# Kernel optimization log

Measured on AMD Instinct MI355X. Metric: run time of the kernel, lower is better.

Reference implementation:

```python
import jax, jax.numpy as jnp
import numpy as np

B, T, N, D = 8, 24, 263, 512
N0, N1 = 32, 64
SEG = 12
LAMBDA_INIT = 0.8 - 0.6 * float(np.exp(-0.3 * (1 - 1)))  # layer_idx=1 -> 0.2


def _ln(x, g, b, eps=1e-5):
    m = jnp.mean(x, axis=-1, keepdims=True)
    v = jnp.var(x, axis=-1, keepdims=True)
    return (x - m) * jax.lax.rsqrt(v + eps) * g + b


def _proj(x, W):
    # 1x1 Conv2d over channel dim == per-position linear, W: [out, in]
    return jnp.einsum('btnd,ed->btne', x, W)


def _forward(x, agg_x0, agg_x1, tmp_map,
             Wq_s, Wk_s, Wv_s, lq1, lk1, lq2, lk2, ln_g, ln_b,
             Wq_a0, Wk_a0, Wv_a0, Wq_a1, Wk_a1, Wv_a1, M0, M1, Wagg, bagg,
             Wq_t, Wk_t, Wv_t, q_agg, Wk_tg, Wv_tg, Wout, bout):
    B, T, N, D = x.shape
    # ---- SpatialDiffAttn: spa_dim=256, heads=4, head_dim=32 (2*32 per head) ----
    H, dh = 4, 32
    q = _proj(x, Wq_s).reshape(B, T, N, H, 2 * dh)
    k = _proj(x, Wk_s).reshape(B, T, N, H, 2 * dh)
    v = _proj(x, Wv_s).reshape(B, T, N, H, 2 * dh)
    q1, q2 = q[..., :dh], q[..., dh:]
    k1, k2 = k[..., :dh], k[..., dh:]
    sc = dh ** -0.5
    # attn11/attn12 share softmax(q1 k1^T); cat([p1@v1, p1@v2]) == p1 @ v_full
    p1 = jax.nn.softmax(jnp.einsum('btnhd,btmhd->bthnm', q1, k1) * sc, axis=-1)
    a1 = jnp.einsum('bthnm,btmhe->btnhe', p1, v)
    p2 = jax.nn.softmax(jnp.einsum('btnhd,btmhd->bthnm', q2, k2) * sc, axis=-1)
    a2 = jnp.einsum('bthnm,btmhe->btnhe', p2, v)
    lam = jnp.exp(jnp.sum(lq1 * lk1)) - jnp.exp(jnp.sum(lq2 * lk2)) + LAMBDA_INIT
    s_x = (_ln(a1 - lam * a2, ln_g, ln_b) * (1.0 - LAMBDA_INIT)).reshape(B, T, N, H * 2 * dh)

    # ---- SpatialAttn aggregated branches (agg_dim=128, heads=2, head_dim=64) ----
    def agg_branch(ax, Wq, Wk, Wv, M):
        Ni = ax.shape[2]
        Ha, dha = 2, 64
        qa = _proj(ax, Wq).reshape(B, T, Ni, Ha, dha)
        ka = _proj(ax, Wk).reshape(B, T, Ni, Ha, dha)
        va = _proj(ax, Wv).reshape(B, T, Ni, Ha, dha)
        pa = jax.nn.softmax(jnp.einsum('btnhd,btmhd->bthnm', qa, ka) * (dha ** -0.5), axis=-1)
        sx = jnp.einsum('bthnm,btmhd->bthnd', pa, va)          # [B,T,Ha,Ni,dha]
        # cls_map = M^T -> pool Ni clusters up to N regions
        return jnp.einsum('mn,bthmd->btnhd', M, sx).reshape(B, T, N, Ha * dha)

    sg = agg_branch(agg_x0, Wq_a0, Wk_a0, Wv_a0, M0) + agg_branch(agg_x1, Wq_a1, Wk_a1, Wv_a1, M1)
    sg = sg @ Wagg.T + bagg

    # ---- TemporalAttn (tmp_dim=128, heads=2, head_dim=64) ----
    Ht, dht = 2, 64
    qt = _proj(x, Wq_t).reshape(B, T, N, Ht, dht)
    kt = _proj(x, Wk_t).reshape(B, T, N, Ht, dht)
    vt = _proj(x, Wv_t).reshape(B, T, N, Ht, dht)
    pt = jax.nn.softmax(jnp.einsum('btnhd,bsnhd->bnhts', qt, kt) * (dht ** -0.5), axis=-1)
    t_x = jnp.einsum('bnhts,bsnhd->btnhd', pt, vt).reshape(B, T, N, Ht * dht)

    # ---- TemporalAttn aggregated (learned query, seg_num=12) ----
    S = q_agg.shape[1]
    qg = q_agg.reshape(N, S, Ht, dht)
    kg = _proj(x, Wk_tg).reshape(B, T, N, Ht, dht)
    vg = _proj(x, Wv_tg).reshape(B, T, N, Ht, dht)
    pg = jax.nn.softmax(jnp.einsum('nshd,btnhd->bnhst', qg, kg) * (dht ** -0.5), axis=-1)
    tgx = jnp.einsum('bnhst,btnhd->bnshd', pg, vg).reshape(B, N, S, Ht * dht)
    tg = jnp.einsum('bnts,bnsd->btnd', tmp_map, tgx)           # [B,T,N,128]

    st = jnp.concatenate([s_x, sg, t_x, tg], axis=-1)          # [B,T,N,640]
    return st @ Wout.T + bout


def setup_inputs() -> dict:
    ks = jax.random.split(jax.random.key(0), 32)
    r = lambda i, shape, s=0.05: (jax.random.normal(ks[i], shape) * s).astype(jnp.float32)
    return dict(
        x=r(0, (B, T, N, D), 1.0),
        agg_x0=r(1, (B, T, N0, D), 1.0),
        agg_x1=r(2, (B, T, N1, D), 1.0),
        tmp_map=jax.random.uniform(ks[3], (B, N, T, SEG), dtype=jnp.float32),
        Wq_s=r(4, (256, D)), Wk_s=r(5, (256, D)), Wv_s=r(6, (256, D)),
        lq1=r(7, (32,), 0.1), lk1=r(8, (32,), 0.1), lq2=r(9, (32,), 0.1), lk2=r(10, (32,), 0.1),
        ln_g=jnp.ones((64,), jnp.float32), ln_b=jnp.zeros((64,), jnp.float32),
        Wq_a0=r(11, (128, D)), Wk_a0=r(12, (128, D)), Wv_a0=r(13, (128, D)),
        Wq_a1=r(14, (128, D)), Wk_a1=r(15, (128, D)), Wv_a1=r(16, (128, D)),
        M0=r(17, (N0, N), 0.1), M1=r(18, (N1, N), 0.1),
        Wagg=r(19, (128, 128)), bagg=jnp.zeros((128,), jnp.float32),
        Wq_t=r(20, (128, D)), Wk_t=r(21, (128, D)), Wv_t=r(22, (128, D)),
        q_agg=r(23, (N, SEG, 128), 1.0),
        Wk_tg=r(24, (128, D)), Wv_tg=r(25, (128, D)),
        Wout=r(26, (D, 640)), bout=jnp.zeros((D,), jnp.float32),
    )


def reference(x, agg_x0, agg_x1, tmp_map,
              Wq_s, Wk_s, Wv_s, lq1, lk1, lq2, lk2, ln_g, ln_b,
              Wq_a0, Wk_a0, Wv_a0, Wq_a1, Wk_a1, Wv_a1, M0, M1, Wagg, bagg,
              Wq_t, Wk_t, Wv_t, q_agg, Wk_tg, Wv_tg, Wout, bout):
    return _forward(x, agg_x0, agg_x1, tmp_map,
                    Wq_s, Wk_s, Wv_s, lq1, lk1, lq2, lk2, ln_g, ln_b,
                    Wq_a0, Wk_a0, Wv_a0, Wq_a1, Wk_a1, Wv_a1, M0, M1, Wagg, bagg,
                    Wq_t, Wk_t, Wv_t, q_agg, Wk_tg, Wv_tg, Wout, bout)
```

## Files before the change

### kernel.cpp

```cpp
#include <hip/hip_runtime.h>

#define NN 263
#define TT 24

typedef __fp16 h2 __attribute__((ext_vector_type(2)));
typedef _Float16 f16x4 __attribute__((ext_vector_type(4)));
typedef _Float16 f16x8 __attribute__((ext_vector_type(8)));
typedef float f32x4 __attribute__((ext_vector_type(4)));

struct WSegs  { const float* p[6]; };
struct WSegsH { const _Float16* p[6]; };
struct CvtSegs { const float* src[11]; _Float16* dst[11]; int cnt8[11]; };

static __device__ __forceinline__ float wred_sum(float v) {
  #pragma unroll
  for (int off = 32; off >= 1; off >>= 1) v += __shfl_xor(v, off, 64);
  return v;
}
static __device__ __forceinline__ float wred_max(float v) {
  #pragma unroll
  for (int off = 32; off >= 1; off >>= 1) v = fmaxf(v, __shfl_xor(v, off, 64));
  return v;
}

__global__ __launch_bounds__(256) void cvt_f16(CvtSegs cs, int nseg, int total8)
{
  const int stride = gridDim.x * 256;
  for (int i = blockIdx.x * 256 + threadIdx.x; i < total8; i += stride) {
    int r = i, s = 0;
    while (s < nseg - 1 && r >= cs.cnt8[s]) { r -= cs.cnt8[s]; ++s; }
    const float* sp = cs.src[s] + (size_t)r * 8;
    float4 a = *(const float4*)sp;
    float4 b = *(const float4*)(sp + 4);
    union { h2 h[4]; f16x8 v; } u;
    u.h[0] = __builtin_amdgcn_cvt_pkrtz(a.x, a.y);
    u.h[1] = __builtin_amdgcn_cvt_pkrtz(a.z, a.w);
    u.h[2] = __builtin_amdgcn_cvt_pkrtz(b.x, b.y);
    u.h[3] = __builtin_amdgcn_cvt_pkrtz(b.z, b.w);
    *(f16x8*)(cs.dst[s] + (size_t)r * 8) = u.v;
  }
}

template<int OUT_HALF>
__global__ __launch_bounds__(256) void gemm_h16(
    const _Float16* __restrict__ A, WSegsH wsg, const float* __restrict__ bias,
    void* __restrict__ Cp, int M, int NT, int K, int ldc)
{
  __shared__ _Float16 As[2][128][40];
  __shared__ _Float16 Bs[2][128][40];
  const int tid  = threadIdx.x;
  const int lane = tid & 63;
  const int wave = tid >> 6;
  const int wr = wave >> 1, wc = wave & 1;

  const int nwg = gridDim.x;
  const int q8 = nwg >> 3, r8 = nwg & 7;
  const int xcd = blockIdx.x & 7, pos = blockIdx.x >> 3;
  const int logical = (xcd < r8 ? xcd * (q8 + 1) : r8 * (q8 + 1) + (xcd - r8) * q8) + pos;
  const int bm = (logical / NT) * 128;
  const int bn = logical - (logical / NT) * NT;
  const _Float16* __restrict__ W = wsg.p[bn];

  const int srow = tid >> 2;
  const int sch  = (tid & 3) * 8;
  const _Float16* aptr[2];
  const _Float16* bptr[2];
  #pragma unroll
  for (int l = 0; l < 2; ++l) {
    int gm = bm + srow + 64 * l; if (gm > M - 1) gm = M - 1;
    aptr[l] = A + (size_t)gm * K + sch;
    bptr[l] = W + (size_t)(srow + 64 * l) * K + sch;
  }

  f32x4 acc[4][4];
  #pragma unroll
  for (int i = 0; i < 4; ++i)
    #pragma unroll
    for (int j = 0; j < 4; ++j) {
      acc[i][j].x = 0.f; acc[i][j].y = 0.f; acc[i][j].z = 0.f; acc[i][j].w = 0.f;
    }

  const int fr = lane & 15;
  const int fk = (lane >> 4) * 8;

  f16x8 av[2], bv[2];
  av[0] = *(const f16x8*)aptr[0]; av[1] = *(const f16x8*)aptr[1];
  bv[0] = *(const f16x8*)bptr[0]; bv[1] = *(const f16x8*)bptr[1];

  int cur = 0;
  for (int k0 = 0; k0 < K; k0 += 32, cur ^= 1) {
    *(f16x8*)&As[cur][srow     ][sch] = av[0];
    *(f16x8*)&As[cur][srow + 64][sch] = av[1];
    *(f16x8*)&Bs[cur][srow     ][sch] = bv[0];
    *(f16x8*)&Bs[cur][srow + 64][sch] = bv[1];
    if (k0 + 32 < K) {
      av[0] = *(const f16x8*)(aptr[0] + k0 + 32);
      av[1] = *(const f16x8*)(aptr[1] + k0 + 32);
      bv[0] = *(const f16x8*)(bptr[0] + k0 + 32);
      bv[1] = *(const f16x8*)(bptr[1] + k0 + 32);
    }
    __syncthreads();

    f16x8 af[4], bf[4];
    #pragma unroll
    for (int mi = 0; mi < 4; ++mi)
      af[mi] = *(const f16x8*)&As[cur][wr * 64 + mi * 16 + fr][fk];
    #pragma unroll
    for (int ni = 0; ni < 4; ++ni)
      bf[ni] = *(const f16x8*)&Bs[cur][wc * 64 + ni * 16 + fr][fk];
    #pragma unroll
    for (int mi = 0; mi < 4; ++mi)
      #pragma unroll
      for (int ni = 0; ni < 4; ++ni)
        acc[mi][ni] = __builtin_amdgcn_mfma_f32_16x16x32_f16(
            af[mi], bf[ni], acc[mi][ni], 0, 0, 0);
  }

  #pragma unroll
  for (int mi = 0; mi < 4; ++mi) {
    int rb = bm + wr * 64 + mi * 16 + (lane >> 4) * 4;
    #pragma unroll
    for (int r = 0; r < 4; ++r) {
      int gm = rb + r;
      if (gm < M) {
        int gn = bn * 128 + wc * 64 + fr;
        #pragma unroll
        for (int ni = 0; ni < 4; ++ni) {
          float v = acc[mi][ni][r];
          if (bias) v += bias[gn + ni * 16];
          if (OUT_HALF) {
            ((_Float16*)Cp)[(size_t)gm * ldc + gn + ni * 16] = (_Float16)v;
          } else {
            ((float*)Cp)[(size_t)gm * ldc + gn + ni * 16] = v;
          }
        }
      }
    }
  }
}

__global__ __launch_bounds__(256) void gemm_nt_mfma(
    const float* __restrict__ A, WSegs ws, const float* __restrict__ bias,
    float* __restrict__ C, int M, int NT, int K, int ldc)
{
  __shared__ _Float16 As[128][40];
  __shared__ _Float16 Bs[128][40];
  const int tid  = threadIdx.x;
  const int lane = tid & 63;
  const int wave = tid >> 6;
  const int wr = wave >> 1, wc = wave & 1;

  const int nwg = gridDim.x;
  const int q8 = nwg >> 3, r8 = nwg & 7;
  const int xcd = blockIdx.x & 7, pos = blockIdx.x >> 3;
  const int logical = (xcd < r8 ? xcd * (q8 + 1) : r8 * (q8 + 1) + (xcd - r8) * q8) + pos;
  const int bm = (logical / NT) * 128;
  const int bn = logical - (logical / NT) * NT;
  const float* __restrict__ W = ws.p[bn];

  const int srow = tid >> 3;
  const int skq  = (tid & 7) * 4;
  const float* aptr[4];
  const float* bptr[4];
  #pragma unroll
  for (int l = 0; l < 4; ++l) {
    int gm = bm + srow + 32 * l; if (gm > M - 1) gm = M - 1;
    aptr[l] = A + (size_t)gm * K + skq;
    bptr[l] = W + (size_t)(srow + 32 * l) * K + skq;
  }

  f32x4 acc[4][4];
  #pragma unroll
  for (int i = 0; i < 4; ++i)
    #pragma unroll
    for (int j = 0; j < 4; ++j) {
      acc[i][j].x = 0.f; acc[i][j].y = 0.f; acc[i][j].z = 0.f; acc[i][j].w = 0.f;
    }

  const int fr = lane & 15;
  const int fk = (lane >> 4) * 8;

  float4 av[4], bv[4];
  #pragma unroll
  for (int l = 0; l < 4; ++l) {
    av[l] = *(const float4*)(aptr[l]);
    bv[l] = *(const float4*)(bptr[l]);
  }

  for (int k0 = 0; k0 < K; k0 += 32) {
    #pragma unroll
    for (int l = 0; l < 4; ++l) {
      f16x4 a4, b4;
      a4.x = (_Float16)av[l].x; a4.y = (_Float16)av[l].y;
      a4.z = (_Float16)av[l].z; a4.w = (_Float16)av[l].w;
      b4.x = (_Float16)bv[l].x; b4.y = (_Float16)bv[l].y;
      b4.z = (_Float16)bv[l].z; b4.w = (_Float16)bv[l].w;
      *(f16x4*)&As[srow + 32 * l][skq] = a4;
      *(f16x4*)&Bs[srow + 32 * l][skq] = b4;
    }
    __syncthreads();

    if (k0 + 32 < K) {
      #pragma unroll
      for (int l = 0; l < 4; ++l) {
        av[l] = *(const float4*)(aptr[l] + k0 + 32);
        bv[l] = *(const float4*)(bptr[l] + k0 + 32);
      }
    }

    f16x8 af[4], bf[4];
    #pragma unroll
    for (int mi = 0; mi < 4; ++mi)
      af[mi] = *(const f16x8*)&As[wr * 64 + mi * 16 + fr][fk];
    #pragma unroll
    for (int ni = 0; ni < 4; ++ni)
      bf[ni] = *(const f16x8*)&Bs[wc * 64 + ni * 16 + fr][fk];
    #pragma unroll
    for (int mi = 0; mi < 4; ++mi)
      #pragma unroll
      for (int ni = 0; ni < 4; ++ni)
        acc[mi][ni] = __builtin_amdgcn_mfma_f32_16x16x32_f16(
            af[mi], bf[ni], acc[mi][ni], 0, 0, 0);
    __syncthreads();
  }

  #pragma unroll
  for (int mi = 0; mi < 4; ++mi) {
    int rb = bm + wr * 64 + mi * 16 + (lane >> 4) * 4;
    #pragma unroll
    for (int r = 0; r < 4; ++r) {
      int gm = rb + r;
      if (gm < M) {
        int gn = bn * 128 + wc * 64 + fr;
        float* crow = C + (size_t)gm * ldc + gn;
        #pragma unroll
        for (int ni = 0; ni < 4; ++ni) {
          float v = acc[mi][ni][r];
          if (bias) v += bias[gn + ni * 16];
          crow[ni * 16] = v;
        }
      }
    }
  }
}

__global__ void lam_kernel(const float* __restrict__ lq1, const float* __restrict__ lk1,
                           const float* __restrict__ lq2, const float* __restrict__ lk2,
                           float* __restrict__ out) {
  int lane = threadIdx.x;
  float v1 = lane < 32 ? lq1[lane] * lk1[lane] : 0.f;
  float v2 = lane < 32 ? lq2[lane] * lk2[lane] : 0.f;
  v1 = wred_sum(v1);
  v2 = wred_sum(v2);
  if (lane == 0) out[0] = expf(v1) - expf(v2) + 0.2f;
}

__global__ __launch_bounds__(512, 2) void diff_attn(
    const float* __restrict__ qkv, float* __restrict__ aout)
{
  __shared__ _Float16 Ks[2][272][40];
  __shared__ h2 Vt[64][148];
  __shared__ h2 Pb[8][16][148];

  const int h  = blockIdx.x & 3;
  const int bt = blockIdx.x >> 2;
  const int tid = threadIdx.x;
  const int lane = tid & 63;
  const int wave = tid >> 6;
  const int fr = lane & 15;
  const int kb = (lane >> 4) * 4;
  const float* base = qkv + (size_t)bt * NN * 768;

  union H4 { f16x4 v; h2 h[2]; };
  union H8 { f16x8 v; h2 h[4]; };

  for (int idx = tid; idx < 272 * 16; idx += 512) {
    int row = idx >> 4, q = idx & 15;
    int sr = row < NN ? row : NN - 1;
    float4 kv = *(const float4*)(base + (size_t)sr * 768 + 256 + h * 64 + q * 4);
    H4 t;
    t.h[0] = __builtin_amdgcn_cvt_pkrtz(kv.x, kv.y);
    t.h[1] = __builtin_amdgcn_cvt_pkrtz(kv.z, kv.w);
    *(f16x4*)&Ks[q >> 3][row][(q & 7) * 4] = t.v;
  }
  for (int idx = tid; idx < 136 * 16; idx += 512) {
    int mp = idx >> 4, dq = (idx & 15) * 4;
    int m0 = 2 * mp, m1 = 2 * mp + 1;
    if (m0 > NN - 1) m0 = NN - 1;
    if (m1 > NN - 1) m1 = NN - 1;
    float4 a = *(const float4*)(base + (size_t)m0 * 768 + 512 + h * 64 + dq);
    float4 b = *(const float4*)(base + (size_t)m1 * 768 + 512 + h * 64 + dq);
    Vt[dq + 0][mp] = __builtin_amdgcn_cvt_pkrtz(a.x, b.x);
    Vt[dq + 1][mp] = __builtin_amdgcn_cvt_pkrtz(a.y, b.y);
    Vt[dq + 2][mp] = __builtin_amdgcn_cvt_pkrtz(a.z, b.z);
    Vt[dq + 3][mp] = __builtin_amdgcn_cvt_pkrtz(a.w, b.w);
  }
  {
    h2 z; z.x = (__fp16)0.f; z.y = (__fp16)0.f;
    for (int idx = tid; idx < 64 * 12; idx += 512)
      Vt[idx / 12][136 + idx % 12] = z;
  }
  {
    h2 z; z.x = (__fp16)0.f; z.y = (__fp16)0.f;
    #pragma unroll
    for (int t = 0; t < 3; ++t) Pb[wave][fr][136 + (kb >> 2) * 3 + t] = z;
  }
  __syncthreads();

  const float scq = 0.17677669529663687f;

  for (int task = wave; task < 34; task += 8) {
    const int chunk = task >> 1;
    const int half  = task & 1;

    int qsrc = chunk * 16 + fr; if (qsrc > NN - 1) qsrc = NN - 1;
    const float* qr = base + (size_t)qsrc * 768 + h * 64 + half * 32 + kb * 2;
    f16x8 qf;
    {
      float4 a = *(const float4*)(qr);
      float4 b = *(const float4*)(qr + 4);
      H8 t;
      t.h[0] = __builtin_amdgcn_cvt_pkrtz(a.x, a.y);
      t.h[1] = __builtin_amdgcn_cvt_pkrtz(a.z, a.w);
      t.h[2] = __builtin_amdgcn_cvt_pkrtz(b.x, b.y);
      t.h[3] = __builtin_amdgcn_cvt_pkrtz(b.z, b.w);
      qf = t.v;
    }

    f32x4 s[17];
    #pragma unroll
    for (int mt = 0; mt < 17; ++mt) {
      f16x8 af = *(const f16x8*)&Ks[half][mt * 16 + fr][kb * 2];
      f32x4 z4 = {0.f, 0.f, 0.f, 0.f};
      s[mt] = __builtin_amdgcn_mfma_f32_16x16x32_f16(af, qf, z4, 0, 0, 0);
    }

    float mx = -1e30f;
    #pragma unroll
    for (int mt = 0; mt < 17; ++mt)
      #pragma unroll
      for (int r = 0; r < 4; ++r) {
        float v = s[mt][r] * scq;
        if (mt * 16 + kb + r >= NN) v = -1e30f;
        s[mt][r] = v;
        mx = fmaxf(mx, v);
      }
    mx = fmaxf(mx, __shfl_xor(mx, 16, 64));
    mx = fmaxf(mx, __shfl_xor(mx, 32, 64));
    float sum = 0.f;
    #pragma unroll
    for (int mt = 0; mt < 17; ++mt)
      #pragma unroll
      for (int r = 0; r < 4; ++r) {
        float p = __expf(s[mt][r] - mx);
        s[mt][r] = p;
        sum += p;
      }
    sum += __shfl_xor(sum, 16, 64);
    sum += __shfl_xor(sum, 32, 64);
    float inv = 1.f / sum;

    #pragma unroll
    for (int mt = 0; mt < 17; ++mt) {
      h2 lo = __builtin_amdgcn_cvt_pkrtz(s[mt][0] * inv, s[mt][1] * inv);
      h2 hi = __builtin_amdgcn_cvt_pkrtz(s[mt][2] * inv, s[mt][3] * inv);
      int kp = 8 * mt + (kb >> 1);
      Pb[wave][fr][kp]     = lo;
      Pb[wave][fr][kp + 1] = hi;
    }

    f32x4 o[4];
    #pragma unroll
    for (int nt = 0; nt < 4; ++nt) {
      o[nt].x = 0.f; o[nt].y = 0.f; o[nt].z = 0.f; o[nt].w = 0.f;
    }
    #pragma unroll
    for (int s9 = 0; s9 < 9; ++s9) {
      f16x8 pa = *(const f16x8*)&Pb[wave][fr][16 * s9 + kb];
      #pragma unroll
      for (int nt = 0; nt < 4; ++nt) {
        f16x8 vb = *(const f16x8*)&Vt[nt * 16 + fr][16 * s9 + kb];
        o[nt] = __builtin_amdgcn_mfma_f32_16x16x32_f16(pa, vb, o[nt], 0, 0, 0);
      }
    }

    float* ab = aout + (size_t)half * (50496ull * 256ull);
    #pragma unroll
    for (int r = 0; r < 4; ++r) {
      int qrow = chunk * 16 + kb + r;
      if (qrow < NN) {
        float* op = ab + ((size_t)(bt * NN + qrow) * 4 + h) * 64;
        #pragma unroll
        for (int nt = 0; nt < 4; ++nt) op[nt * 16 + fr] = o[nt][r];
      }
    }
  }
}

__global__ __launch_bounds__(256) void diff_ln(
    const float* __restrict__ a1, const float* __restrict__ a2,
    const float* __restrict__ lamp,
    const float* __restrict__ g, const float* __restrict__ b,
    _Float16* __restrict__ st)
{
  const int btn = blockIdx.x;
  const int lane = threadIdx.x & 63;
  const int h = threadIdx.x >> 6;
  const float lam = lamp[0];
  size_t off = ((size_t)btn * 4 + h) * 64 + lane;
  float y = a1[off] - lam * a2[off];
  float mean = wred_sum(y) * (1.f / 64.f);
  float t = y - mean;
  float var = wred_sum(t * t) * (1.f / 64.f);
  float r = rsqrtf(var + 1e-5f);
  st[(size_t)btn * 640 + h * 64 + lane] = (_Float16)((t * r * g[lane] + b[lane]) * 0.8f);
}

__global__ __launch_bounds__(256) void temporal_attn(
    const float* __restrict__ qkvt, _Float16* __restrict__ st)
{
  __shared__ float qs[48][68];
  __shared__ float kt[48][68];
  __shared__ float vt[48][68];
  __shared__ float Ss[48][28];
  const int b = blockIdx.x / NN;
  const int n = blockIdx.x % NN;
  const int tid = threadIdx.x;
  const int lane = tid & 63;
  const int wave = tid >> 6;

  for (int idx = tid; idx < 48 * 16; idx += 256) {
    int row = idx >> 4, dq = (idx & 15) * 4;
    int h = row / 24, t = row - h * 24;
    const float* g = qkvt + ((size_t)(b * TT + t) * NN + n) * 640 + h * 64 + dq;
    *(float4*)&qs[row][dq] = *(const float4*)(g);
    *(float4*)&kt[row][dq] = *(const float4*)(g + 128);
    *(float4*)&vt[row][dq] = *(const float4*)(g + 256);
  }
  __syncthreads();

  for (int idx = tid; idx < 48 * 24; idx += 256) {
    int row = idx / 24, s = idx - row * 24;
    int krow = (row >= 24 ? 24 : 0) + s;
    float a0 = 0.f, a1 = 0.f, a2 = 0.f, a3 = 0.f;
    #pragma unroll
    for (int dq = 0; dq < 64; dq += 4) {
      float4 q = *(const float4*)&qs[row][dq];
      float4 k = *(const float4*)&kt[krow][dq];
      a0 = fmaf(q.x, k.x, a0);
      a1 = fmaf(q.y, k.y, a1);
      a2 = fmaf(q.z, k.z, a2);
      a3 = fmaf(q.w, k.w, a3);
    }
    Ss[row][s] = ((a0 + a1) + (a2 + a3)) * 0.125f;
  }
  __syncthreads();

  for (int r = wave; r < 48; r += 4) {
    float v = lane < 24 ? Ss[r][lane] : -1e30f;
    float mx = wred_max(v);
    float p = lane < 24 ? __expf(v - mx) : 0.f;
    float inv = 1.f / wred_sum(p);
    if (lane < 24) Ss[r][lane] = p * inv;
  }
  __syncthreads();

  for (int idx = tid; idx < 48 * 16; idx += 256) {
    int row = idx >> 4, dq = (idx & 15) * 4;
    int h = row / 24, t = row - h * 24;
    int bs = h * 24;
    float ax = 0.f, ay = 0.f, az = 0.f, aw = 0.f;
    #pragma unroll
    for (int s = 0; s < 24; ++s) {
      float p = Ss[row][s];
      float4 v = *(const float4*)&vt[bs + s][dq];
      ax = fmaf(p, v.x, ax);
      ay = fmaf(p, v.y, ay);
      az = fmaf(p, v.z, az);
      aw = fmaf(p, v.w, aw);
    }
    union { h2 h[2]; f16x4 v; } o2;
    o2.h[0] = __builtin_amdgcn_cvt_pkrtz(ax, ay);
    o2.h[1] = __builtin_amdgcn_cvt_pkrtz(az, aw);
    *(f16x4*)(st + ((size_t)(b * TT + t) * NN + n) * 640 + 384 + h * 64 + dq) = o2.v;
  }
}

__global__ __launch_bounds__(256) void tglobal_attn(
    const float* __restrict__ qkvt, const float* __restrict__ q_agg,
    const float* __restrict__ tmp_map, _Float16* __restrict__ st)
{
  __shared__ float qg[24][68];
  __shared__ float kg[48][68];
  __shared__ float vg[48][68];
  __shared__ float Sg[24][28];
  __shared__ float tgx[12][128];
  const int b = blockIdx.x / NN;
  const int n = blockIdx.x % NN;
  const int tid = threadIdx.x;
  const int lane = tid & 63;
  const int wave = tid >> 6;

  for (int idx = tid; idx < 48 * 16; idx += 256) {
    int row = idx >> 4, dq = (idx & 15) * 4;
    int h = row / 24, t = row - h * 24;
    const float* g = qkvt + ((size_t)(b * TT + t) * NN + n) * 640 + 384 + h * 64 + dq;
    *(float4*)&kg[row][dq] = *(const float4*)(g);
    *(float4*)&vg[row][dq] = *(const float4*)(g + 128);
  }
  for (int idx = tid; idx < 24 * 16; idx += 256) {
    int row = idx >> 4, dq = (idx & 15) * 4;
    int h = row / 12, s = row - h * 12;
    *(float4*)&qg[row][dq] =
        *(const float4*)(q_agg + ((size_t)n * 12 + s) * 128 + h * 64 + dq);
  }
  __syncthreads();

  for (int idx = tid; idx < 24 * 24; idx += 256) {
    int row = idx / 24, t = idx - row * 24;
    int krow = (row >= 12 ? 24 : 0) + t;
    float a0 = 0.f, a1 = 0.f, a2 = 0.f, a3 = 0.f;
    #pragma unroll
    for (int dq = 0; dq < 64; dq += 4) {
      float4 q = *(const float4*)&qg[row][dq];
      float4 k = *(const float4*)&kg[krow][dq];
      a0 = fmaf(q.x, k.x, a0);
      a1 = fmaf(q.y, k.y, a1);
      a2 = fmaf(q.z, k.z, a2);
      a3 = fmaf(q.w, k.w, a3);
    }
    Sg[row][t] = ((a0 + a1) + (a2 + a3)) * 0.125f;
  }
  __syncthreads();

  for (int r = wave; r < 24; r += 4) {
    float v = lane < 24 ? Sg[r][lane] : -1e30f;
    float mx = wred_max(v);
    float p = lane < 24 ? __expf(v - mx) : 0.f;
    float inv = 1.f / wred_sum(p);
    if (lane < 24) Sg[r][lane] = p * inv;
  }
  __syncthreads();

  for (int idx = tid; idx < 24 * 16; idx += 256) {
    int row = idx >> 4, dq = (idx & 15) * 4;
    int h = row / 12, s = row - h * 12;
    int bt_ = h * 24;
    float ax = 0.f, ay = 0.f, az = 0.f, aw = 0.f;
    #pragma unroll
    for (int t = 0; t < 24; ++t) {
      float p = Sg[row][t];
      float4 v = *(const float4*)&vg[bt_ + t][dq];
      ax = fmaf(p, v.x, ax);
      ay = fmaf(p, v.y, ay);
      az = fmaf(p, v.z, az);
      aw = fmaf(p, v.w, aw);
    }
    float4 o = {ax, ay, az, aw};
    *(float4*)&tgx[s][h * 64 + dq] = o;
  }
  __syncthreads();

  for (int idx = tid; idx < 24 * 32; idx += 256) {
    int t = idx >> 5, cq = (idx & 31) * 4;
    const float* tm = tmp_map + ((size_t)(b * NN + n) * TT + t) * 12;
    float ax = 0.f, ay = 0.f, az = 0.f, aw = 0.f;
    #pragma unroll
    for (int s = 0; s < 12; ++s) {
      float m = tm[s];
      float4 v = *(const float4*)&tgx[s][cq];
      ax = fmaf(m, v.x, ax);
      ay = fmaf(m, v.y, ay);
      az = fmaf(m, v.z, az);
      aw = fmaf(m, v.w, aw);
    }
    union { h2 h[2]; f16x4 v; } o2;
    o2.h[0] = __builtin_amdgcn_cvt_pkrtz(ax, ay);
    o2.h[1] = __builtin_amdgcn_cvt_pkrtz(az, aw);
    *(f16x4*)(st + ((size_t)(b * TT + t) * NN + n) * 640 + 512 + cq) = o2.v;
  }
}

__global__ __launch_bounds__(256) void agg_attn(
    const float* __restrict__ qkva, float* __restrict__ sx, int Ni)
{
  __shared__ float kT[64 * 64];
  __shared__ float vl[64 * 64];
  const int h = blockIdx.x & 1;
  const int bt = blockIdx.x >> 1;
  const int tid = threadIdx.x;
  const int lane = tid & 63;
  const int wave = tid >> 6;
  for (int idx = tid; idx < Ni * 64; idx += 256) {
    int m = idx >> 6, d = idx & 63;
    size_t row = (size_t)(bt * Ni + m) * 384;
    kT[d * Ni + m] = qkva[row + 128 + h * 64 + d];
    vl[m * 64 + d] = qkva[row + 256 + h * 64 + d];
  }
  __syncthreads();
  int mc = lane < Ni ? lane : Ni - 1;
  bool valid = lane < Ni;
  for (int n = wave; n < Ni; n += 4) {
    float qv = qkva[(size_t)(bt * Ni + n) * 384 + h * 64 + lane];
    float sc_ = 0.f;
    #pragma unroll
    for (int d = 0; d < 64; ++d) {
      float qd = __shfl(qv, d, 64);
      sc_ = fmaf(qd, kT[d * Ni + mc], sc_);
    }
    sc_ *= 0.125f;
    float mx = wred_max(valid ? sc_ : -1e30f);
    float p = valid ? __expf(sc_ - mx) : 0.f;
    float inv = 1.f / wred_sum(p);
    float o = 0.f;
    for (int m = 0; m < Ni; ++m) {
      float pm = __shfl(p, m, 64);
      o = fmaf(pm, vl[m * 64 + lane], o);
    }
    sx[(size_t)(bt * Ni + n) * 128 + h * 64 + lane] = o * inv;
  }
}

__global__ __launch_bounds__(256) void mmap_kernel(
    const float* __restrict__ sx0, const float* __restrict__ sx1,
    const float* __restrict__ M0, const float* __restrict__ M1,
    _Float16* __restrict__ sg)
{
  __shared__ float sS[96][128];
  __shared__ float Mc[96][88];
  const int bt = blockIdx.x;
  const int chunk = blockIdx.y;
  const int tid = threadIdx.x;
  const int nbase = chunk * 88;

  for (int idx = tid; idx < 96 * 32; idx += 256) {
    int m = idx >> 5, c4 = (idx & 31) * 4;
    float4 v = (m < 32)
        ? *(const float4*)(sx0 + ((size_t)(bt * 32 + m) * 128 + c4))
        : *(const float4*)(sx1 + ((size_t)(bt * 64 + (m - 32)) * 128 + c4));
    *(float4*)&sS[m][c4] = v;
  }
  for (int idx = tid; idx < 96 * 88; idx += 256) {
    int m = idx / 88, nl = idx - m * 88;
    int n = nbase + nl; if (n > NN - 1) n = NN - 1;
    Mc[m][nl] = (m < 32) ? M0[m * NN + n] : M1[(m - 32) * NN + n];
  }
  __syncthreads();

  for (int idx = tid; idx < 352; idx += 256) {
    const int n0 = (idx >> 5) * 8;
    const int c4 = (idx & 31) * 4;
    f32x4 acc[8];
    #pragma unroll
    for (int j = 0; j < 8; ++j) {
      acc[j].x = 0.f; acc[j].y = 0.f; acc[j].z = 0.f; acc[j].w = 0.f;
    }
    #pragma unroll 4
    for (int m = 0; m < 96; ++m) {
      float4 sv = *(const float4*)&sS[m][c4];
      float mj[8];
      *(float4*)&mj[0] = *(const float4*)&Mc[m][n0];
      *(float4*)&mj[4] = *(const float4*)&Mc[m][n0 + 4];
      #pragma unroll
      for (int j = 0; j < 8; ++j) {
        acc[j].x = fmaf(mj[j], sv.x, acc[j].x);
        acc[j].y = fmaf(mj[j], sv.y, acc[j].y);
        acc[j].z = fmaf(mj[j], sv.z, acc[j].z);
        acc[j].w = fmaf(mj[j], sv.w, acc[j].w);
      }
    }
    #pragma unroll
    for (int j = 0; j < 8; ++j) {
      int n = nbase + n0 + j;
      if (n < NN) {
        union { h2 h[2]; f16x4 v; } o;
        o.h[0] = __builtin_amdgcn_cvt_pkrtz(acc[j].x, acc[j].y);
        o.h[1] = __builtin_amdgcn_cvt_pkrtz(acc[j].z, acc[j].w);
        *(f16x4*)(sg + ((size_t)bt * NN + n) * 128 + c4) = o.v;
      }
    }
  }
}

extern "C" void kernel_launch(void* const* d_in, const int* in_sizes, int n_in,
                              void* d_out, int out_size, void* d_ws, size_t ws_size,
                              hipStream_t stream)
{
  const float* x       = (const float*)d_in[0];
  const float* agg_x0  = (const float*)d_in[1];
  const float* agg_x1  = (const float*)d_in[2];
  const float* tmp_map = (const float*)d_in[3];
  const float* Wq_s = (const float*)d_in[4];
  const float* Wk_s = (const float*)d_in[5];
  const float* Wv_s = (const float*)d_in[6];
  const float* lq1 = (const float*)d_in[7];
  const float* lk1 = (const float*)d_in[8];
  const float* lq2 = (const float*)d_in[9];
  const float* lk2 = (const float*)d_in[10];
  const float* ln_g = (const float*)d_in[11];
  const float* ln_b = (const float*)d_in[12];
  const float* Wq_a0 = (const float*)d_in[13];
  const float* Wk_a0 = (const float*)d_in[14];
  const float* Wv_a0 = (const float*)d_in[15];
  const float* Wq_a1 = (const float*)d_in[16];
  const float* Wk_a1 = (const float*)d_in[17];
  const float* Wv_a1 = (const float*)d_in[18];
  const float* M0   = (const float*)d_in[19];
  const float* M1   = (const float*)d_in[20];
  const float* Wagg = (const float*)d_in[21];
  const float* bagg = (const float*)d_in[22];
  const float* Wq_t = (const float*)d_in[23];
  const float* Wk_t = (const float*)d_in[24];
  const float* Wv_t = (const float*)d_in[25];
  const float* q_agg = (const float*)d_in[26];
  const float* Wk_tg = (const float*)d_in[27];
  const float* Wv_tg = (const float*)d_in[28];
  const float* Wout  = (const float*)d_in[29];
  const float* bout  = (const float*)d_in[30];
  float* ws  = (float*)d_ws;
  float* out = (float*)d_out;

  const size_t o_lam  = 1114112;
  const size_t o_A    = 1114128;
  const size_t o_qkvt = o_A + 38780928;
  const size_t o_B    = o_qkvt + 32317440;

  float* lamp  = ws + o_lam;
  float* qkv_s = ws + o_A;
  _Float16* st_h = (_Float16*)(ws + o_A);
  float* qkvt  = ws + o_qkvt;
  _Float16* x_h = (_Float16*)(ws + o_B);
  float* a1    = ws + o_B;
  float* qkva0 = ws + o_B;
  float* qkva1 = qkva0 + 2359296;
  float* sx0   = qkva0 + 7077888;
  float* sx1   = qkva0 + 7864320;
  _Float16* sg_h = (_Float16*)(qkva0 + 9437184);
  _Float16* Wh  = (_Float16*)ws;

  hipLaunchKernelGGL(lam_kernel, dim3(1), dim3(64), 0, stream, lq1, lk1, lq2, lk2, lamp);

  CvtSegs cs;
  cs.src[0] = x;      cs.dst[0] = x_h;          cs.cnt8[0] = 25853952 / 8;
  cs.src[1] = Wq_s;   cs.dst[1] = Wh + 0;       cs.cnt8[1] = 131072 / 8;
  cs.src[2] = Wk_s;   cs.dst[2] = Wh + 131072;  cs.cnt8[2] = 131072 / 8;
  cs.src[3] = Wv_s;   cs.dst[3] = Wh + 262144;  cs.cnt8[3] = 131072 / 8;
  cs.src[4] = Wq_t;   cs.dst[4] = Wh + 393216;  cs.cnt8[4] = 65536 / 8;
  cs.src[5] = Wk_t;   cs.dst[5] = Wh + 458752;  cs.cnt8[5] = 65536 / 8;
  cs.src[6] = Wv_t;   cs.dst[6] = Wh + 524288;  cs.cnt8[6] = 65536 / 8;
  cs.src[7] = Wk_tg;  cs.dst[7] = Wh + 589824;  cs.cnt8[7] = 65536 / 8;
  cs.src[8] = Wv_tg;  cs.dst[8] = Wh + 655360;  cs.cnt8[8] = 65536 / 8;
  cs.src[9] = Wagg;   cs.dst[9] = Wh + 720896;  cs.cnt8[9] = 16384 / 8;
  cs.src[10] = Wout;  cs.dst[10] = Wh + 737280; cs.cnt8[10] = 327680 / 8;
  hipLaunchKernelGGL(cvt_f16, dim3(2048), dim3(256), 0, stream, cs, 11, 3364864);

  const int Mx = 50496;

  WSegsH wqkv; wqkv.p[0] = Wh; wqkv.p[1] = Wh + 65536;
  wqkv.p[2] = Wh + 131072; wqkv.p[3] = Wh + 196608;
  wqkv.p[4] = Wh + 262144; wqkv.p[5] = Wh + 327680;
  hipLaunchKernelGGL((gemm_h16<0>), dim3(395 * 6), dim3(256), 0, stream,
                     x_h, wqkv, (const float*)nullptr, (void*)qkv_s, Mx, 6, 512, 768);

  WSegsH wt; wt.p[0] = Wh + 393216; wt.p[1] = Wh + 458752; wt.p[2] = Wh + 524288;
  wt.p[3] = Wh + 589824; wt.p[4] = Wh + 655360; wt.p[5] = Wh + 393216;
  hipLaunchKernelGGL((gemm_h16<0>), dim3(395 * 5), dim3(256), 0, stream,
                     x_h, wt, (const float*)nullptr, (void*)qkvt, Mx, 5, 512, 640);

  hipLaunchKernelGGL(diff_attn, dim3(768), dim3(512), 0, stream, qkv_s, a1);
  hipLaunchKernelGGL(diff_ln, dim3(Mx), dim3(256), 0, stream,
                     a1, a1 + 12926976, lamp, ln_g, ln_b, st_h);
  hipLaunchKernelGGL(temporal_attn, dim3(8 * NN), dim3(256), 0, stream, qkvt, st_h);
  hipLaunchKernelGGL(tglobal_attn, dim3(8 * NN), dim3(256), 0, stream, qkvt, q_agg, tmp_map, st_h);

  WSegs wa0; wa0.p[0] = Wq_a0; wa0.p[1] = Wk_a0; wa0.p[2] = Wv_a0;
  wa0.p[3] = wa0.p[4] = wa0.p[5] = Wq_a0;
  hipLaunchKernelGGL(gemm_nt_mfma, dim3(48 * 3), dim3(256), 0, stream,
                     agg_x0, wa0, (const float*)nullptr, qkva0, 6144, 3, 512, 384);
  WSegs wa1; wa1.p[0] = Wq_a1; wa1.p[1] = Wk_a1; wa1.p[2] = Wv_a1;
  wa1.p[3] = wa1.p[4] = wa1.p[5] = Wq_a1;
  hipLaunchKernelGGL(gemm_nt_mfma, dim3(96 * 3), dim3(256), 0, stream,
                     agg_x1, wa1, (const float*)nullptr, qkva1, 12288, 3, 512, 384);

  hipLaunchKernelGGL(agg_attn, dim3(384), dim3(256), 0, stream, qkva0, sx0, 32);
  hipLaunchKernelGGL(agg_attn, dim3(384), dim3(256), 0, stream, qkva1, sx1, 64);
  hipLaunchKernelGGL(mmap_kernel, dim3(192, 3), dim3(256), 0, stream, sx0, sx1, M0, M1, sg_h);

  WSegsH wag; wag.p[0] = Wh + 720896;
  wag.p[1] = wag.p[2] = wag.p[3] = wag.p[4] = wag.p[5] = wag.p[0];
  hipLaunchKernelGGL((gemm_h16<1>), dim3(395 * 1), dim3(256), 0, stream,
                     sg_h, wag, bagg, (void*)(st_h + 256), Mx, 1, 128, 640);

  WSegsH wo; wo.p[0] = Wh + 737280; wo.p[1] = Wh + 737280 + 81920;
  wo.p[2] = Wh + 737280 + 163840; wo.p[3] = Wh + 737280 + 245760;
  wo.p[4] = wo.p[5] = wo.p[0];
  hipLaunchKernelGGL((gemm_h16<0>), dim3(395 * 4), dim3(256), 0, stream,
                     st_h, wo, bout, (void*)out, Mx, 4, 640, 512);
}
```

Baseline: 894.1 us.

## Store QKV projections and attention outputs in fp16, restructure aggregated attention

The spatial and temporal QKV GEMMs now write fp16 intermediates instead of fp32, and the diff attention, LN, temporal and global attention kernels read fp16 directly, dropping in-kernel conversions. This halves the intermediate memory traffic between these stages. The agg_attn kernel is also rewritten to stage Q/K/V in shared memory and compute scores, softmax and PV with vectorised loops. There are minor softmax tweaks too: split max and sum accumulators and a vectorised P store. The cost is fp16 rounding of intermediates, plus more shared memory per block in agg_attn.

```diff
diff --git a/kernel.cpp b/kernel.cpp
--- a/kernel.cpp
+++ b/kernel.cpp
@@ -256,7 +256,7 @@
 }
 
 __global__ __launch_bounds__(512, 2) void diff_attn(
-    const float* __restrict__ qkv, float* __restrict__ aout)
+    const _Float16* __restrict__ qkv, _Float16* __restrict__ aout)
 {
   __shared__ _Float16 Ks[2][272][40];
   __shared__ h2 Vt[64][148];
@@ -269,36 +269,34 @@
   const int wave = tid >> 6;
   const int fr = lane & 15;
   const int kb = (lane >> 4) * 4;
-  const float* base = qkv + (size_t)bt * NN * 768;
-
-  union H4 { f16x4 v; h2 h[2]; };
-  union H8 { f16x8 v; h2 h[4]; };
-
-  for (int idx = tid; idx < 272 * 16; idx += 512) {
-    int row = idx >> 4, q = idx & 15;
+  const _Float16* base = qkv + (size_t)bt * NN * 768;
+
+  for (int idx = tid; idx < 272 * 8; idx += 512) {
+    int row = idx >> 3, c = idx & 7;
     int sr = row < NN ? row : NN - 1;
-    float4 kv = *(const float4*)(base + (size_t)sr * 768 + 256 + h * 64 + q * 4);
-    H4 t;
-    t.h[0] = __builtin_amdgcn_cvt_pkrtz(kv.x, kv.y);
-    t.h[1] = __builtin_amdgcn_cvt_pkrtz(kv.z, kv.w);
-    *(f16x4*)&Ks[q >> 3][row][(q & 7) * 4] = t.v;
-  }
-  for (int idx = tid; idx < 136 * 16; idx += 512) {
-    int mp = idx >> 4, dq = (idx & 15) * 4;
-    int m0 = 2 * mp, m1 = 2 * mp + 1;
-    if (m0 > NN - 1) m0 = NN - 1;
-    if (m1 > NN - 1) m1 = NN - 1;
-    float4 a = *(const float4*)(base + (size_t)m0 * 768 + 512 + h * 64 + dq);
-    float4 b = *(const float4*)(base + (size_t)m1 * 768 + 512 + h * 64 + dq);
-    Vt[dq + 0][mp] = __builtin_amdgcn_cvt_pkrtz(a.x, b.x);
-    Vt[dq + 1][mp] = __builtin_amdgcn_cvt_pkrtz(a.y, b.y);
-    Vt[dq + 2][mp] = __builtin_amdgcn_cvt_pkrtz(a.z, b.z);
-    Vt[dq + 3][mp] = __builtin_amdgcn_cvt_pkrtz(a.w, b.w);
+    f16x8 kv = *(const f16x8*)(base + (size_t)sr * 768 + 256 + h * 64 + c * 8);
+    *(f16x8*)&Ks[c >> 2][row][(c & 3) * 8] = kv;
   }
   {
-    h2 z; z.x = (__fp16)0.f; z.y = (__fp16)0.f;
-    for (int idx = tid; idx < 64 * 12; idx += 512)
-      Vt[idx / 12][136 + idx % 12] = z;
+    const ushort* vb = (const ushort*)(base + 512 + h * 64);
+    for (int idx = tid; idx < 64 * 37; idx += 512) {
+      int d = idx & 63, kp0 = (idx >> 6) * 4;
+      union { ushort u[8]; f16x8 v; } w;
+      #pragma unroll
+      for (int i = 0; i < 4; ++i) {
+        int kp = kp0 + i;
+        ushort lo = 0, hi = 0;
+        if (kp < 136) {
+          int m0 = 2 * kp, m1 = 2 * kp + 1;
+          if (m0 > NN - 1) m0 = NN - 1;
+          if (m1 > NN - 1) m1 = NN - 1;
+          lo = vb[(size_t)m0 * 768 + d];
+          hi = vb[(size_t)m1 * 768 + d];
+        }
+        w.u[2 * i] = lo; w.u[2 * i + 1] = hi;
+      }
+      *(f16x8*)&Vt[d][kp0] = w.v;
+    }
   }
   {
     h2 z; z.x = (__fp16)0.f; z.y = (__fp16)0.f;
@@ -314,18 +312,7 @@
     const int half  = task & 1;
 
     int qsrc = chunk * 16 + fr; if (qsrc > NN - 1) qsrc = NN - 1;
-    const float* qr = base + (size_t)qsrc * 768 + h * 64 + half * 32 + kb * 2;
-    f16x8 qf;
-    {
-      float4 a = *(const float4*)(qr);
-      float4 b = *(const float4*)(qr + 4);
-      H8 t;
-      t.h[0] = __builtin_amdgcn_cvt_pkrtz(a.x, a.y);
-      t.h[1] = __builtin_amdgcn_cvt_pkrtz(a.z, a.w);
-      t.h[2] = __builtin_amdgcn_cvt_pkrtz(b.x, b.y);
-      t.h[3] = __builtin_amdgcn_cvt_pkrtz(b.z, b.w);
-      qf = t.v;
-    }
+    f16x8 qf = *(const f16x8*)(base + (size_t)qsrc * 768 + h * 64 + half * 32 + kb * 2);
 
     f32x4 s[17];
     #pragma unroll
@@ -335,7 +322,7 @@
       s[mt] = __builtin_amdgcn_mfma_f32_16x16x32_f16(af, qf, z4, 0, 0, 0);
     }
 
-    float mx = -1e30f;
+    float mx4[4] = {-1e30f, -1e30f, -1e30f, -1e30f};
     #pragma unroll
     for (int mt = 0; mt < 17; ++mt)
       #pragma unroll
@@ -343,30 +330,31 @@
         float v = s[mt][r] * scq;
         if (mt * 16 + kb + r >= NN) v = -1e30f;
         s[mt][r] = v;
-        mx = fmaxf(mx, v);
-      }
+        mx4[r] = fmaxf(mx4[r], v);
+      }
+    float mx = fmaxf(fmaxf(mx4[0], mx4[1]), fmaxf(mx4[2], mx4[3]));
     mx = fmaxf(mx, __shfl_xor(mx, 16, 64));
     mx = fmaxf(mx, __shfl_xor(mx, 32, 64));
-    float sum = 0.f;
+    float sm4[4] = {0.f, 0.f, 0.f, 0.f};
     #pragma unroll
     for (int mt = 0; mt < 17; ++mt)
       #pragma unroll
       for (int r = 0; r < 4; ++r) {
         float p = __expf(s[mt][r] - mx);
         s[mt][r] = p;
-        sum += p;
-      }
+        sm4[r] += p;
+      }
+    float sum = (sm4[0] + sm4[1]) + (sm4[2] + sm4[3]);
     sum += __shfl_xor(sum, 16, 64);
     sum += __shfl_xor(sum, 32, 64);
     float inv = 1.f / sum;
 
     #pragma unroll
     for (int mt = 0; mt < 17; ++mt) {
-      h2 lo = __builtin_amdgcn_cvt_pkrtz(s[mt][0] * inv, s[mt][1] * inv);
-      h2 hi = __builtin_amdgcn_cvt_pkrtz(s[mt][2] * inv, s[mt][3] * inv);
-      int kp = 8 * mt + (kb >> 1);
-      Pb[wave][fr][kp]     = lo;
-      Pb[wave][fr][kp + 1] = hi;
+      union { h2 h[2]; f16x4 v; } pw;
+      pw.h[0] = __builtin_amdgcn_cvt_pkrtz(s[mt][0] * inv, s[mt][1] * inv);
+      pw.h[1] = __builtin_amdgcn_cvt_pkrtz(s[mt][2] * inv, s[mt][3] * inv);
+      *(f16x4*)&Pb[wave][fr][8 * mt + (kb >> 1)] = pw.v;
     }
 
     f32x4 o[4];
@@ -379,26 +367,26 @@
       f16x8 pa = *(const f16x8*)&Pb[wave][fr][16 * s9 + kb];
       #pragma unroll
       for (int nt = 0; nt < 4; ++nt) {
-        f16x8 vb = *(const f16x8*)&Vt[nt * 16 + fr][16 * s9 + kb];
-        o[nt] = __builtin_amdgcn_mfma_f32_16x16x32_f16(pa, vb, o[nt], 0, 0, 0);
-      }
-    }
-
-    float* ab = aout + (size_t)half * (50496ull * 256ull);
+        f16x8 vb2 = *(const f16x8*)&Vt[nt * 16 + fr][16 * s9 + kb];
+        o[nt] = __builtin_amdgcn_mfma_f32_16x16x32_f16(pa, vb2, o[nt], 0, 0, 0);
+      }
+    }
+
+    _Float16* ab = aout + (size_t)half * (50496ull * 256ull);
     #pragma unroll
     for (int r = 0; r < 4; ++r) {
       int qrow = chunk * 16 + kb + r;
       if (qrow < NN) {
-        float* op = ab + ((size_t)(bt * NN + qrow) * 4 + h) * 64;
+        _Float16* op = ab + ((size_t)(bt * NN + qrow) * 4 + h) * 64;
         #pragma unroll
-        for (int nt = 0; nt < 4; ++nt) op[nt * 16 + fr] = o[nt][r];
+        for (int nt = 0; nt < 4; ++nt) op[nt * 16 + fr] = (_Float16)o[nt][r];
       }
     }
   }
 }
 
 __global__ __launch_bounds__(256) void diff_ln(
-    const float* __restrict__ a1, const float* __restrict__ a2,
+    const _Float16* __restrict__ a1, const _Float16* __restrict__ a2,
     const float* __restrict__ lamp,
     const float* __restrict__ g, const float* __restrict__ b,
     _Float16* __restrict__ st)
@@ -408,7 +396,7 @@
   const int h = threadIdx.x >> 6;
   const float lam = lamp[0];
   size_t off = ((size_t)btn * 4 + h) * 64 + lane;
-  float y = a1[off] - lam * a2[off];
+  float y = (float)a1[off] - lam * (float)a2[off];
   float mean = wred_sum(y) * (1.f / 64.f);
   float t = y - mean;
   float var = wred_sum(t * t) * (1.f / 64.f);
@@ -417,7 +405,7 @@
 }
 
 __global__ __launch_bounds__(256) void temporal_attn(
-    const float* __restrict__ qkvt, _Float16* __restrict__ st)
+    const _Float16* __restrict__ qkvt, _Float16* __restrict__ st)
 {
   __shared__ float qs[48][68];
   __shared__ float kt[48][68];
@@ -432,10 +420,16 @@
   for (int idx = tid; idx < 48 * 16; idx += 256) {
     int row = idx >> 4, dq = (idx & 15) * 4;
     int h = row / 24, t = row - h * 24;
-    const float* g = qkvt + ((size_t)(b * TT + t) * NN + n) * 640 + h * 64 + dq;
-    *(float4*)&qs[row][dq] = *(const float4*)(g);
-    *(float4*)&kt[row][dq] = *(const float4*)(g + 128);
-    *(float4*)&vt[row][dq] = *(const float4*)(g + 256);
+    const _Float16* g = qkvt + ((size_t)(b * TT + t) * NN + n) * 640 + h * 64 + dq;
+    f16x4 a = *(const f16x4*)(g);
+    f16x4 k = *(const f16x4*)(g + 128);
+    f16x4 v = *(const f16x4*)(g + 256);
+    float4 fa = {(float)a.x, (float)a.y, (float)a.z, (float)a.w};
+    float4 fk = {(float)k.x, (float)k.y, (float)k.z, (float)k.w};
+    float4 fv = {(float)v.x, (float)v.y, (float)v.z, (float)v.w};
+    *(float4*)&qs[row][dq] = fa;
+    *(float4*)&kt[row][dq] = fk;
+    *(float4*)&vt[row][dq] = fv;
   }
   __syncthreads();
 
@@ -487,7 +481,7 @@
 }
 
 __global__ __launch_bounds__(256) void tglobal_attn(
-    const float* __restrict__ qkvt, const float* __restrict__ q_agg,
+    const _Float16* __restrict__ qkvt, const float* __restrict__ q_agg,
     const float* __restrict__ tmp_map, _Float16* __restrict__ st)
 {
   __shared__ float qg[24][68];
@@ -504,9 +498,13 @@
   for (int idx = tid; idx < 48 * 16; idx += 256) {
     int row = idx >> 4, dq = (idx & 15) * 4;
     int h = row / 24, t = row - h * 24;
-    const float* g = qkvt + ((size_t)(b * TT + t) * NN + n) * 640 + 384 + h * 64 + dq;
-    *(float4*)&kg[row][dq] = *(const float4*)(g);
-    *(float4*)&vg[row][dq] = *(const float4*)(g + 128);
+    const _Float16* g = qkvt + ((size_t)(b * TT + t) * NN + n) * 640 + 384 + h * 64 + dq;
+    f16x4 k = *(const f16x4*)(g);
+    f16x4 v = *(const f16x4*)(g + 128);
+    float4 fk = {(float)k.x, (float)k.y, (float)k.z, (float)k.w};
+    float4 fv = {(float)v.x, (float)v.y, (float)v.z, (float)v.w};
+    *(float4*)&kg[row][dq] = fk;
+    *(float4*)&vg[row][dq] = fv;
   }
   for (int idx = tid; idx < 24 * 16; idx += 256) {
     int row = idx >> 4, dq = (idx & 15) * 4;
@@ -582,42 +580,65 @@
 }
 
 __global__ __launch_bounds__(256) void agg_attn(
-    const float* __restrict__ qkva, float* __restrict__ sx, int Ni)
-{
-  __shared__ float kT[64 * 64];
-  __shared__ float vl[64 * 64];
+    const float* __restrict__ qkva, float* __restrict__ sx, int Ni, int lg)
+{
+  __shared__ float qa[64][68];
+  __shared__ float ka[64][68];
+  __shared__ float va[64][68];
+  __shared__ float Ss[64][68];
   const int h = blockIdx.x & 1;
   const int bt = blockIdx.x >> 1;
   const int tid = threadIdx.x;
   const int lane = tid & 63;
   const int wave = tid >> 6;
-  for (int idx = tid; idx < Ni * 64; idx += 256) {
-    int m = idx >> 6, d = idx & 63;
-    size_t row = (size_t)(bt * Ni + m) * 384;
-    kT[d * Ni + m] = qkva[row + 128 + h * 64 + d];
-    vl[m * 64 + d] = qkva[row + 256 + h * 64 + d];
-  }
-  __syncthreads();
-  int mc = lane < Ni ? lane : Ni - 1;
-  bool valid = lane < Ni;
-  for (int n = wave; n < Ni; n += 4) {
-    float qv = qkva[(size_t)(bt * Ni + n) * 384 + h * 64 + lane];
-    float sc_ = 0.f;
-    #pragma unroll
-    for (int d = 0; d < 64; ++d) {
-      float qd = __shfl(qv, d, 64);
-      sc_ = fmaf(qd, kT[d * Ni + mc], sc_);
-    }
-    sc_ *= 0.125f;
-    float mx = wred_max(valid ? sc_ : -1e30f);
-    float p = valid ? __expf(sc_ - mx) : 0.f;
+
+  for (int idx = tid; idx < Ni * 16; idx += 256) {
+    int m = idx >> 4, dq = (idx & 15) * 4;
+    const float* r = qkva + (size_t)(bt * Ni + m) * 384 + h * 64 + dq;
+    *(float4*)&qa[m][dq] = *(const float4*)(r);
+    *(float4*)&ka[m][dq] = *(const float4*)(r + 128);
+    *(float4*)&va[m][dq] = *(const float4*)(r + 256);
+  }
+  __syncthreads();
+
+  for (int idx = tid; idx < Ni * Ni; idx += 256) {
+    int n = idx >> lg, m = idx & (Ni - 1);
+    float a0 = 0.f, a1 = 0.f, a2 = 0.f, a3 = 0.f;
+    #pragma unroll
+    for (int dq = 0; dq < 64; dq += 4) {
+      float4 q = *(const float4*)&qa[n][dq];
+      float4 k = *(const float4*)&ka[m][dq];
+      a0 = fmaf(q.x, k.x, a0);
+      a1 = fmaf(q.y, k.y, a1);
+      a2 = fmaf(q.z, k.z, a2);
+      a3 = fmaf(q.w, k.w, a3);
+    }
+    Ss[n][m] = ((a0 + a1) + (a2 + a3)) * 0.125f;
+  }
+  __syncthreads();
+
+  for (int r = wave; r < Ni; r += 4) {
+    float v = lane < Ni ? Ss[r][lane] : -1e30f;
+    float mx = wred_max(v);
+    float p = lane < Ni ? __expf(v - mx) : 0.f;
     float inv = 1.f / wred_sum(p);
-    float o = 0.f;
+    if (lane < Ni) Ss[r][lane] = p * inv;
+  }
+  __syncthreads();
+
+  for (int idx = tid; idx < Ni * 16; idx += 256) {
+    int n = idx >> 4, dq = (idx & 15) * 4;
+    float ax = 0.f, ay = 0.f, az = 0.f, aw = 0.f;
     for (int m = 0; m < Ni; ++m) {
-      float pm = __shfl(p, m, 64);
-      o = fmaf(pm, vl[m * 64 + lane], o);
-    }
-    sx[(size_t)(bt * Ni + n) * 128 + h * 64 + lane] = o * inv;
+      float p = Ss[n][m];
+      float4 v = *(const float4*)&va[m][dq];
+      ax = fmaf(p, v.x, ax);
+      ay = fmaf(p, v.y, ay);
+      az = fmaf(p, v.z, az);
+      aw = fmaf(p, v.w, aw);
+    }
+    float4 o = {ax, ay, az, aw};
+    *(float4*)(sx + (size_t)(bt * Ni + n) * 128 + h * 64 + dq) = o;
   }
 }
 
@@ -726,11 +747,11 @@
   const size_t o_B    = o_qkvt + 32317440;
 
   float* lamp  = ws + o_lam;
-  float* qkv_s = ws + o_A;
-  _Float16* st_h = (_Float16*)(ws + o_A);
-  float* qkvt  = ws + o_qkvt;
+  _Float16* qkv_h  = (_Float16*)(ws + o_A);
+  _Float16* st_h   = (_Float16*)(ws + o_A);
+  _Float16* qkvt_h = (_Float16*)(ws + o_qkvt);
   _Float16* x_h = (_Float16*)(ws + o_B);
-  float* a1    = ws + o_B;
+  _Float16* a1_h = (_Float16*)(ws + o_B);
   float* qkva0 = ws + o_B;
   float* qkva1 = qkva0 + 2359296;
   float* sx0   = qkva0 + 7077888;
@@ -759,19 +780,19 @@
   WSegsH wqkv; wqkv.p[0] = Wh; wqkv.p[1] = Wh + 65536;
   wqkv.p[2] = Wh + 131072; wqkv.p[3] = Wh + 196608;
   wqkv.p[4] = Wh + 262144; wqkv.p[5] = Wh + 327680;
-  hipLaunchKernelGGL((gemm_h16<0>), dim3(395 * 6), dim3(256), 0, stream,
-                     x_h, wqkv, (const float*)nullptr, (void*)qkv_s, Mx, 6, 512, 768);
+  hipLaunchKernelGGL((gemm_h16<1>), dim3(395 * 6), dim3(256), 0, stream,
+                     x_h, wqkv, (const float*)nullptr, (void*)qkv_h, Mx, 6, 512, 768);
 
   WSegsH wt; wt.p[0] = Wh + 393216; wt.p[1] = Wh + 458752; wt.p[2] = Wh + 524288;
   wt.p[3] = Wh + 589824; wt.p[4] = Wh + 655360; wt.p[5] = Wh + 393216;
-  hipLaunchKernelGGL((gemm_h16<0>), dim3(395 * 5), dim3(256), 0, stream,
-                     x_h, wt, (const float*)nullptr, (void*)qkvt, Mx, 5, 512, 640);
-
-  hipLaunchKernelGGL(diff_attn, dim3(768), dim3(512), 0, stream, qkv_s, a1);
+  hipLaunchKernelGGL((gemm_h16<1>), dim3(395 * 5), dim3(256), 0, stream,
+                     x_h, wt, (const float*)nullptr, (void*)qkvt_h, Mx, 5, 512, 640);
+
+  hipLaunchKernelGGL(diff_attn, dim3(768), dim3(512), 0, stream, qkv_h, a1_h);
   hipLaunchKernelGGL(diff_ln, dim3(Mx), dim3(256), 0, stream,
-                     a1, a1 + 12926976, lamp, ln_g, ln_b, st_h);
-  hipLaunchKernelGGL(temporal_attn, dim3(8 * NN), dim3(256), 0, stream, qkvt, st_h);
-  hipLaunchKernelGGL(tglobal_attn, dim3(8 * NN), dim3(256), 0, stream, qkvt, q_agg, tmp_map, st_h);
+                     a1_h, a1_h + 12926976, lamp, ln_g, ln_b, st_h);
+  hipLaunchKernelGGL(temporal_attn, dim3(8 * NN), dim3(256), 0, stream, qkvt_h, st_h);
+  hipLaunchKernelGGL(tglobal_attn, dim3(8 * NN), dim3(256), 0, stream, qkvt_h, q_agg, tmp_map, st_h);
 
   WSegs wa0; wa0.p[0] = Wq_a0; wa0.p[1] = Wk_a0; wa0.p[2] = Wv_a0;
   wa0.p[3] = wa0.p[4] = wa0.p[5] = Wq_a0;
@@ -782,8 +803,8 @@
   hipLaunchKernelGGL(gemm_nt_mfma, dim3(96 * 3), dim3(256), 0, stream,
                      agg_x1, wa1, (const float*)nullptr, qkva1, 12288, 3, 512, 384);
 
-  hipLaunchKernelGGL(agg_attn, dim3(384), dim3(256), 0, stream, qkva0, sx0, 32);
-  hipLaunchKernelGGL(agg_attn, dim3(384), dim3(256), 0, stream, qkva1, sx1, 64);
+  hipLaunchKernelGGL(agg_attn, dim3(384), dim3(256), 0, stream, qkva0, sx0, 32, 5);
+  hipLaunchKernelGGL(agg_attn, dim3(384), dim3(256), 0, stream, qkva1, sx1, 64, 6);
   hipLaunchKernelGGL(mmap_kernel, dim3(192, 3), dim3(256), 0, stream, sx0, sx1, M0, M1, sg_h);
 
   WSegsH wag; wag.p[0] = Wh + 720896;
```

Measured after the change: 839.3 us. 1.07x faster.
